# Kernel tuning notes

Hardware: AMD Instinct MI355X
Metric: run time of the kernel (lower is better)

## Reference

```python
import jax, jax.numpy as jnp
import numpy as np

V = 128      # vocab size (pad=0, sos=1, eos=2)
E = 128      # embed_dim == LSTM hidden
L = 2        # rnn_layers
B = 8192     # batch (num_samples)
T = 128      # token sequence length incl. sos/eos
PAD, SOS, EOS = 0, 1, 2


def setup_inputs() -> dict:
    key = jax.random.key(0)
    ks = jax.random.split(key, 9)
    s = 1.0 / np.sqrt(E)
    state = jax.random.normal(ks[0], (B, E), dtype=jnp.float32)
    tokens = jax.random.randint(ks[1], (B, T), 3, V)
    tokens = tokens.at[:, 0].set(SOS).at[:, -1].set(EOS)
    tok_embed = jax.random.normal(ks[2], (V, E), dtype=jnp.float32)
    W_ih = jax.random.uniform(ks[3], (L, 4 * E, E), minval=-s, maxval=s, dtype=jnp.float32)
    W_hh = jax.random.uniform(ks[4], (L, 4 * E, E), minval=-s, maxval=s, dtype=jnp.float32)
    b_ih = jax.random.uniform(ks[5], (L, 4 * E), minval=-s, maxval=s, dtype=jnp.float32)
    b_hh = jax.random.uniform(ks[6], (L, 4 * E), minval=-s, maxval=s, dtype=jnp.float32)
    W_out = jax.random.uniform(ks[7], (V, E), minval=-s, maxval=s, dtype=jnp.float32)
    b_out = jax.random.uniform(ks[8], (V,), minval=-s, maxval=s, dtype=jnp.float32)
    return {"state": state, "tokens": tokens, "tok_embed": tok_embed,
            "W_ih": W_ih, "W_hh": W_hh, "b_ih": b_ih, "b_hh": b_hh,
            "W_out": W_out, "b_out": b_out}


def _lstm(x, h0, c0, W_ih, W_hh, b_ih, b_hh):
    # x: [T, B, E] time-major; h0/c0: [L, B, E]. Gate order i,f,g,o (torch).
    n_layers = W_ih.shape[0]
    hs, cs = [], []
    for l in range(n_layers):
        Wih, Whh = W_ih[l], W_hh[l]
        b = b_ih[l] + b_hh[l]
        def step(carry, xt, Wih=Wih, Whh=Whh, b=b):
            h, c = carry
            g = xt @ Wih.T + h @ Whh.T + b            # [B, 4E]
            i, f, gg, o = jnp.split(g, 4, axis=-1)
            c = jax.nn.sigmoid(f) * c + jax.nn.sigmoid(i) * jnp.tanh(gg)
            h = jax.nn.sigmoid(o) * jnp.tanh(c)
            return (h, c), h
        (h, c), x = jax.lax.scan(step, (h0[l], c0[l]), x)
        hs.append(h)
        cs.append(c)
    return x, jnp.stack(hs), jnp.stack(cs)


def reference(state, tokens, tok_embed, W_ih, W_hh, b_ih, b_hh, W_out, b_out):
    b, e = state.shape
    n_layers = W_ih.shape[0]
    zeros = jnp.zeros((n_layers, b, e), dtype=state.dtype)
    # get_init_state: one-step LSTM over state.unsqueeze(0)
    _, h0, c0 = _lstm(state[None], zeros, zeros, W_ih, W_hh, b_ih, b_hh)
    # get_likelihood (all sequences same length -> dense, no pad tokens)
    x = tok_embed[tokens.T]                               # [T, B, E]
    out, _, _ = _lstm(x, h0, c0, W_ih, W_hh, b_ih, b_hh)  # [T, B, E]
    logits = out[:-1] @ W_out.T + b_out                   # [T-1, B, V]
    targets = tokens.T[1:]                                # [T-1, B]
    lp = jax.nn.log_softmax(logits, axis=-1)
    nll = -jnp.take_along_axis(lp, targets[..., None], axis=-1)[..., 0]
    mask = (targets != PAD).astype(nll.dtype)             # ignore_index=pad
    ll = -jnp.sum(nll * mask, axis=0)[:, None]            # [B, 1]
    return ll
```

## Files before the change

### kernel.cpp

```cpp
#include <hip/hip_runtime.h>
#include <hip/hip_bf16.h>


typedef __bf16 bf16x8 __attribute__((ext_vector_type(8)));
typedef __bf16 bf16x4 __attribute__((ext_vector_type(4)));
typedef float  f32x4  __attribute__((ext_vector_type(4)));

#define LOG2E 1.4426950408889634f
#define LN2   0.6931471805599453f

static __device__ __bf16 g_emb1[128 * 512];

__device__ __forceinline__ float frcp(float x) {
#if __has_builtin(__builtin_amdgcn_rcpf)
  return __builtin_amdgcn_rcpf(x);
#else
  return 1.0f / x;
#endif
}
__device__ __forceinline__ float fexp2(float x) {
#if __has_builtin(__builtin_amdgcn_exp2f)
  return __builtin_amdgcn_exp2f(x);
#else
  return exp2f(x);
#endif
}
__device__ __forceinline__ float flog2(float x) {
#if __has_builtin(__builtin_amdgcn_logf)
  return __builtin_amdgcn_logf(x);
#else
  return log2f(x);
#endif
}

__global__ void prep_emb1(const float* __restrict__ emb, const float* __restrict__ Wih,
                          const float* __restrict__ bih, const float* __restrict__ bhh) {
  __shared__ float embS[128 * 128];
  __shared__ float wS[32 * 128];
  const int tid = threadIdx.x, bc = blockIdx.x;
  for (int i = tid; i < 128 * 32; i += 512) ((f32x4*)embS)[i] = ((const f32x4*)emb)[i];
  for (int i = tid; i < 32 * 32; i += 512)
    ((f32x4*)wS)[i] = ((const f32x4*)(Wih + bc * 32 * 128))[i];
  __syncthreads();
  const int v = tid & 127, c0 = (tid >> 7) * 8;
  const int rot = v & 31;
#pragma unroll
  for (int j = 0; j < 8; ++j) {
    int c = c0 + j;
    float s = 0.f;
    for (int k = 0; k < 128; ++k) {
      int kk = (k + rot) & 127;
      s += embS[v * 128 + kk] * wS[c * 128 + kk];
    }
    int col = bc * 32 + c;
    float sc = ((col >> 7) == 2) ? 2.0f * LOG2E : LOG2E;
    g_emb1[v * 512 + col] = (__bf16)((s + bih[col] + bhh[col]) * sc);
  }
}

__global__ __launch_bounds__(512, 2) void lstm_ll(
    const float* __restrict__ state, const int* __restrict__ tokens,
    const float* __restrict__ W_ih, const float* __restrict__ W_hh,
    const float* __restrict__ b_ih, const float* __restrict__ b_hh,
    const float* __restrict__ W_out, const float* __restrict__ b_out,
    float* __restrict__ out) {
  __shared__ __align__(16) __bf16 wih2L[512 * 128];
  __shared__ __align__(16) __bf16 h1L[2][32 * 128];
  __shared__ __align__(16) __bf16 h2L[32 * 128];
  __shared__ unsigned char tokL[128][32];
  __shared__ float wsum[8][32];
  __shared__ float llL[32];

  const int tid  = threadIdx.x;
  const int w    = tid >> 6;
  const int lane = tid & 63;
  const int lr   = lane & 15;
  const int lh   = lane >> 4;
  const int b0   = blockIdx.x * 32;
  const int col  = w * 16 + lr;
  const int koff = lh * 8;
  const int e0   = w * 16 + lh * 4;
  const float gscA[4] = {LOG2E, LOG2E, 2.0f * LOG2E, LOG2E};
  const int sw = (lr & 7) << 3;

  for (int i = tid; i < 512 * 16; i += 512) {
    int row = i >> 4, e = (i & 15) * 8;
    const float* p = W_ih + 512 * 128 + row * 128 + e;
    float sc = gscA[row >> 7];
    f32x4 x0 = *(const f32x4*)p, x1 = *(const f32x4*)(p + 4);
    bf16x8 v;
#pragma unroll
    for (int j = 0; j < 4; ++j) { v[j] = (__bf16)(x0[j] * sc); v[4 + j] = (__bf16)(x1[j] * sc); }
    *(bf16x8*)(wih2L + row * 128 + (e ^ ((row & 7) << 3))) = v;
  }
  for (int i = tid; i < 32 * 128; i += 512) {
    int r = i & 31, t = i >> 5;
    tokL[t][r] = (unsigned char)tokens[(b0 + r) * 128 + t];
  }
  if (tid < 32) llL[tid] = 0.0f;

  auto ldw8s = [&](const float* p, float sc) -> bf16x8 {
    f32x4 x0 = *(const f32x4*)p, x1 = *(const f32x4*)(p + 4);
    bf16x8 v;
#pragma unroll
    for (int j = 0; j < 4; ++j) { v[j] = (__bf16)(x0[j] * sc); v[4 + j] = (__bf16)(x1[j] * sc); }
    return v;
  };

  bf16x8 whh1[4][4], whh2[4][4], woutF[4];
#pragma unroll
  for (int kc = 0; kc < 4; ++kc) {
#pragma unroll
    for (int gg = 0; gg < 4; ++gg) {
      whh1[kc][gg] = ldw8s(W_hh + (gg * 128 + col) * 128 + kc * 32 + koff, gscA[gg]);
      whh2[kc][gg] = ldw8s(W_hh + 512 * 128 + (gg * 128 + col) * 128 + kc * 32 + koff, gscA[gg]);
    }
    woutF[kc] = ldw8s(W_out + col * 128 + kc * 32 + koff, LOG2E);
  }
  f32x4 bias2v4[4], bo4;
#pragma unroll
  for (int gg = 0; gg < 4; ++gg)
#pragma unroll
    for (int j = 0; j < 4; ++j)
      bias2v4[gg][j] = (b_ih[512 + gg * 128 + e0 + j] + b_hh[512 + gg * 128 + e0 + j]) * gscA[gg];
#pragma unroll
  for (int j = 0; j < 4; ++j) bo4[j] = b_out[e0 + j] * LOG2E;

  float c1[2][4] = {}, c2[2][4] = {};

  auto ldB = [&](const __bf16* buf, int nf, int kc) -> bf16x8 {
    return *(const bf16x8*)(buf + (nf * 16 + lr) * 128 + ((kc * 32 + koff) ^ sw));
  };

  f32x4 acc[4][2];
  auto zacc = [&]() {
#pragma unroll
    for (int gg = 0; gg < 4; ++gg)
#pragma unroll
      for (int nf = 0; nf < 2; ++nf) acc[gg][nf] = f32x4{0.f, 0.f, 0.f, 0.f};
  };

  auto elem = [&](const f32x4* b4, float (&c)[2][4], __bf16* hout) {
#pragma unroll
    for (int nf = 0; nf < 2; ++nf) {
      bf16x4 hp;
#pragma unroll
      for (int j = 0; j < 4; ++j) {
        float gi = acc[0][nf][j] + b4[0][j];
        float gf = acc[1][nf][j] + b4[1][j];
        float gc = acc[2][nf][j] + b4[2][j];
        float go = acc[3][nf][j] + b4[3][j];
        float sf = frcp(1.f + fexp2(-gf));
        float si = frcp(1.f + fexp2(-gi));
        float tg = 1.f - 2.f * frcp(fexp2(gc) + 1.f);
        float cc = sf * c[nf][j] + si * tg;
        c[nf][j] = cc;
        float so = frcp(1.f + fexp2(-go));
        float tc = 1.f - 2.f * frcp(fexp2(2.f * LOG2E * cc) + 1.f);
        hp[j] = (__bf16)(so * tc);
      }
      int b = nf * 16 + lr;
      *(bf16x4*)(hout + b * 128 + (e0 ^ ((b & 7) << 3))) = hp;
    }
  };
  const f32x4 zf4 = {0.f, 0.f, 0.f, 0.f};
  const f32x4 zb4[4] = {zf4, zf4, zf4, zf4};

  __syncthreads();

  bf16x4 gv[2][4];
  auto gather = [&](int t) {
#pragma unroll
    for (int nf = 0; nf < 2; ++nf) {
      int tk = (int)tokL[t][nf * 16 + lr];
      const __bf16* pp = g_emb1 + tk * 512 + e0;
#pragma unroll
      for (int gg = 0; gg < 4; ++gg) gv[nf][gg] = *(const bf16x4*)(pp + gg * 128);
    }
  };
  gather(0);

  {
    zacc();
#pragma unroll
    for (int kc = 0; kc < 4; ++kc) {
      bf16x8 s0 = ldw8s(state + (size_t)(b0 + lr) * 128 + kc * 32 + koff, 1.0f);
      bf16x8 s1 = ldw8s(state + (size_t)(b0 + 16 + lr) * 128 + kc * 32 + koff, 1.0f);
#pragma unroll
      for (int gg = 0; gg < 4; ++gg) {
        bf16x8 a = ldw8s(W_ih + (gg * 128 + col) * 128 + kc * 32 + koff, gscA[gg]);
        acc[gg][0] = __builtin_amdgcn_mfma_f32_16x16x32_bf16(a, s0, acc[gg][0], 0, 0, 0);
        acc[gg][1] = __builtin_amdgcn_mfma_f32_16x16x32_bf16(a, s1, acc[gg][1], 0, 0, 0);
      }
    }
    f32x4 bias1v4[4];
#pragma unroll
    for (int gg = 0; gg < 4; ++gg)
#pragma unroll
      for (int j = 0; j < 4; ++j)
        bias1v4[gg][j] = (b_ih[gg * 128 + e0 + j] + b_hh[gg * 128 + e0 + j]) * gscA[gg];
    elem(bias1v4, c1, h1L[0]);
    __syncthreads();
    zacc();
#pragma unroll
    for (int kc = 0; kc < 4; ++kc) {
      bf16x8 x0 = ldB(h1L[0], 0, kc), x1 = ldB(h1L[0], 1, kc);
#pragma unroll
      for (int gg = 0; gg < 4; ++gg) {
        bf16x8 a = *(const bf16x8*)(wih2L + (gg * 128 + col) * 128 + ((kc * 32 + koff) ^ sw));
        acc[gg][0] = __builtin_amdgcn_mfma_f32_16x16x32_bf16(a, x0, acc[gg][0], 0, 0, 0);
        acc[gg][1] = __builtin_amdgcn_mfma_f32_16x16x32_bf16(a, x1, acc[gg][1], 0, 0, 0);
      }
    }
    elem(bias2v4, c2, h2L);
    __syncthreads();
  }

  f32x4 lvA, lvB;

#pragma unroll 1
  for (int t = 0; t <= 127; ++t) {
    const bool act = (t < 127), pend = (t > 0);
    const __bf16* h1p = h1L[t & 1];
    __bf16* h1c = h1L[(t & 1) ^ 1];

    if (pend) {
      f32x4 la0 = zf4, la1 = zf4;
#pragma unroll
      for (int kc = 0; kc < 4; ++kc) {
        bf16x8 y0 = ldB(h2L, 0, kc), y1 = ldB(h2L, 1, kc);
        la0 = __builtin_amdgcn_mfma_f32_16x16x32_bf16(woutF[kc], y0, la0, 0, 0, 0);
        la1 = __builtin_amdgcn_mfma_f32_16x16x32_bf16(woutF[kc], y1, la1, 0, 0, 0);
      }
      lvA = la0 + bo4;
      lvB = la1 + bo4;
    }
    if (act) {
      zacc();
#pragma unroll
      for (int kc = 0; kc < 4; ++kc) {
        bf16x8 p0 = ldB(h1p, 0, kc), p1 = ldB(h1p, 1, kc);
#pragma unroll
        for (int gg = 0; gg < 4; ++gg) {
          acc[gg][0] = __builtin_amdgcn_mfma_f32_16x16x32_bf16(whh1[kc][gg], p0, acc[gg][0], 0, 0, 0);
          acc[gg][1] = __builtin_amdgcn_mfma_f32_16x16x32_bf16(whh1[kc][gg], p1, acc[gg][1], 0, 0, 0);
        }
      }
#pragma unroll
      for (int nf = 0; nf < 2; ++nf)
#pragma unroll
        for (int gg = 0; gg < 4; ++gg)
#pragma unroll
          for (int j = 0; j < 4; ++j) acc[gg][nf][j] += (float)gv[nf][gg][j];
    }
    if (pend) {
      float s0 = fexp2(lvA[0]) + fexp2(lvA[1]) + fexp2(lvA[2]) + fexp2(lvA[3]);
      float s1 = fexp2(lvB[0]) + fexp2(lvB[1]) + fexp2(lvB[2]) + fexp2(lvB[3]);
      s0 += __shfl_xor(s0, 16); s0 += __shfl_xor(s0, 32);
      s1 += __shfl_xor(s1, 16); s1 += __shfl_xor(s1, 32);
      if (lh == 0) { wsum[w][lr] = s0; wsum[w][16 + lr] = s1; }
    }
    if (act) elem(zb4, c1, h1c);
    __syncthreads();

    if (act) {
      if (t + 1 < 127) gather(t + 1);
      zacc();
#pragma unroll
      for (int kc = 0; kc < 4; ++kc) {
        bf16x8 x0 = ldB(h1c, 0, kc), x1 = ldB(h1c, 1, kc);
        bf16x8 y0 = ldB(h2L, 0, kc), y1 = ldB(h2L, 1, kc);
#pragma unroll
        for (int gg = 0; gg < 4; ++gg) {
          bf16x8 a = *(const bf16x8*)(wih2L + (gg * 128 + col) * 128 + ((kc * 32 + koff) ^ sw));
          acc[gg][0] = __builtin_amdgcn_mfma_f32_16x16x32_bf16(a, x0, acc[gg][0], 0, 0, 0);
          acc[gg][1] = __builtin_amdgcn_mfma_f32_16x16x32_bf16(a, x1, acc[gg][1], 0, 0, 0);
          acc[gg][0] = __builtin_amdgcn_mfma_f32_16x16x32_bf16(whh2[kc][gg], y0, acc[gg][0], 0, 0, 0);
          acc[gg][1] = __builtin_amdgcn_mfma_f32_16x16x32_bf16(whh2[kc][gg], y1, acc[gg][1], 0, 0, 0);
        }
      }
    }
    if (pend) {
#pragma unroll
      for (int nf = 0; nf < 2; ++nf) {
        int r = nf * 16 + lr;
        int tgt = (int)tokL[t][r];
        if ((tgt >> 4) == w && ((tgt >> 2) & 3) == lh) {
          int j = tgt & 3;
          const f32x4& lv = nf ? lvB : lvA;
          float lvs = (j & 2) ? ((j & 1) ? lv[3] : lv[2]) : ((j & 1) ? lv[1] : lv[0]);
          float S = 0.f;
#pragma unroll
          for (int ww = 0; ww < 8; ++ww) S += wsum[ww][r];
          llL[r] += lvs - flog2(S);
        }
      }
    }
    __syncthreads();

    if (act) elem(bias2v4, c2, h2L);
    __syncthreads();
  }

  if (tid < 32) out[b0 + tid] = llL[tid] * LN2;
}

extern "C" void kernel_launch(void* const* d_in, const int* in_sizes, int n_in,
                              void* d_out, int out_size, void* d_ws, size_t ws_size,
                              hipStream_t stream) {
  const float* state  = (const float*)d_in[0];
  const int*   tokens = (const int*)d_in[1];
  const float* emb    = (const float*)d_in[2];
  const float* Wih    = (const float*)d_in[3];
  const float* Whh    = (const float*)d_in[4];
  const float* bih    = (const float*)d_in[5];
  const float* bhh    = (const float*)d_in[6];
  const float* Wout   = (const float*)d_in[7];
  const float* bout   = (const float*)d_in[8];
  float* out = (float*)d_out;

  prep_emb1<<<16, 512, 0, stream>>>(emb, Wih, bih, bhh);
  lstm_ll<<<256, 512, 0, stream>>>(state, tokens, Wih, Whh, bih, bhh, Wout, bout, out);
}
```

Before: 1.128 ms.

## Reschedule LSTM time loop to two barriers per step and rotate-swizzle LDS

Restructures the per-timestep loop into a skewed pipeline. Layer-2 elementwise, softmax partial sums and layer-1 recurrence now share one barrier phase, and the layer-2 GEMM is fused with the output-logit GEMM so both read the h2 tile once. This drops the number of __syncthreads per step from three to two and overlaps independent work. It also replaces the XOR LDS swizzle with a row-rotation swizzle over 16 rows to cut bank conflicts. The pipeline adds an extra loop iteration and shifts token indexing, which raises the risk of off-by-one errors.

```diff
diff --git a/kernel.cpp b/kernel.cpp
--- a/kernel.cpp
+++ b/kernel.cpp
@@ -31,6 +31,10 @@
 #else
   return log2f(x);
 #endif
+}
+
+__device__ __forceinline__ int hoff(int row, int e) {
+  return row * 128 + ((e + ((row & 15) << 3)) & 127);
 }
 
 __global__ void prep_emb1(const float* __restrict__ emb, const float* __restrict__ Wih,
@@ -81,7 +85,6 @@
   const int koff = lh * 8;
   const int e0   = w * 16 + lh * 4;
   const float gscA[4] = {LOG2E, LOG2E, 2.0f * LOG2E, LOG2E};
-  const int sw = (lr & 7) << 3;
 
   for (int i = tid; i < 512 * 16; i += 512) {
     int row = i >> 4, e = (i & 15) * 8;
@@ -91,7 +94,7 @@
     bf16x8 v;
 #pragma unroll
     for (int j = 0; j < 4; ++j) { v[j] = (__bf16)(x0[j] * sc); v[4 + j] = (__bf16)(x1[j] * sc); }
-    *(bf16x8*)(wih2L + row * 128 + (e ^ ((row & 7) << 3))) = v;
+    *(bf16x8*)(wih2L + hoff(row, e)) = v;
   }
   for (int i = tid; i < 32 * 128; i += 512) {
     int r = i & 31, t = i >> 5;
@@ -129,7 +132,7 @@
   float c1[2][4] = {}, c2[2][4] = {};
 
   auto ldB = [&](const __bf16* buf, int nf, int kc) -> bf16x8 {
-    return *(const bf16x8*)(buf + (nf * 16 + lr) * 128 + ((kc * 32 + koff) ^ sw));
+    return *(const bf16x8*)(buf + hoff(nf * 16 + lr, kc * 32 + koff));
   };
 
   f32x4 acc[4][2];
@@ -160,7 +163,7 @@
         hp[j] = (__bf16)(so * tc);
       }
       int b = nf * 16 + lr;
-      *(bf16x4*)(hout + b * 128 + (e0 ^ ((b & 7) << 3))) = hp;
+      *(bf16x4*)(hout + hoff(b, e0)) = hp;
     }
   };
   const f32x4 zf4 = {0.f, 0.f, 0.f, 0.f};
@@ -199,15 +202,15 @@
 #pragma unroll
       for (int j = 0; j < 4; ++j)
         bias1v4[gg][j] = (b_ih[gg * 128 + e0 + j] + b_hh[gg * 128 + e0 + j]) * gscA[gg];
-    elem(bias1v4, c1, h1L[0]);
+    elem(bias1v4, c1, h1L[1]);
     __syncthreads();
     zacc();
 #pragma unroll
     for (int kc = 0; kc < 4; ++kc) {
-      bf16x8 x0 = ldB(h1L[0], 0, kc), x1 = ldB(h1L[0], 1, kc);
+      bf16x8 x0 = ldB(h1L[1], 0, kc), x1 = ldB(h1L[1], 1, kc);
 #pragma unroll
       for (int gg = 0; gg < 4; ++gg) {
-        bf16x8 a = *(const bf16x8*)(wih2L + (gg * 128 + col) * 128 + ((kc * 32 + koff) ^ sw));
+        bf16x8 a = *(const bf16x8*)(wih2L + hoff(gg * 128 + col, kc * 32 + koff));
         acc[gg][0] = __builtin_amdgcn_mfma_f32_16x16x32_bf16(a, x0, acc[gg][0], 0, 0, 0);
         acc[gg][1] = __builtin_amdgcn_mfma_f32_16x16x32_bf16(a, x1, acc[gg][1], 0, 0, 0);
       }
@@ -219,72 +222,47 @@
   f32x4 lvA, lvB;
 
 #pragma unroll 1
-  for (int t = 0; t <= 127; ++t) {
-    const bool act = (t < 127), pend = (t > 0);
-    const __bf16* h1p = h1L[t & 1];
-    __bf16* h1c = h1L[(t & 1) ^ 1];
-
-    if (pend) {
-      f32x4 la0 = zf4, la1 = zf4;
-#pragma unroll
-      for (int kc = 0; kc < 4; ++kc) {
-        bf16x8 y0 = ldB(h2L, 0, kc), y1 = ldB(h2L, 1, kc);
-        la0 = __builtin_amdgcn_mfma_f32_16x16x32_bf16(woutF[kc], y0, la0, 0, 0, 0);
-        la1 = __builtin_amdgcn_mfma_f32_16x16x32_bf16(woutF[kc], y1, la1, 0, 0, 0);
-      }
-      lvA = la0 + bo4;
-      lvB = la1 + bo4;
-    }
-    if (act) {
-      zacc();
-#pragma unroll
-      for (int kc = 0; kc < 4; ++kc) {
-        bf16x8 p0 = ldB(h1p, 0, kc), p1 = ldB(h1p, 1, kc);
-#pragma unroll
-        for (int gg = 0; gg < 4; ++gg) {
-          acc[gg][0] = __builtin_amdgcn_mfma_f32_16x16x32_bf16(whh1[kc][gg], p0, acc[gg][0], 0, 0, 0);
-          acc[gg][1] = __builtin_amdgcn_mfma_f32_16x16x32_bf16(whh1[kc][gg], p1, acc[gg][1], 0, 0, 0);
-        }
-      }
-#pragma unroll
-      for (int nf = 0; nf < 2; ++nf)
-#pragma unroll
-        for (int gg = 0; gg < 4; ++gg)
-#pragma unroll
-          for (int j = 0; j < 4; ++j) acc[gg][nf][j] += (float)gv[nf][gg][j];
-    }
-    if (pend) {
+  for (int t = 0; t <= 128; ++t) {
+    const bool doL1 = (t <= 126);
+    const bool doE2 = (t >= 1) && (t <= 127);
+    const bool doSM = (t >= 2);
+    const bool doLG = (t >= 1) && (t <= 127);
+
+    if (doE2) elem(bias2v4, c2, h2L);
+    if (doSM) {
       float s0 = fexp2(lvA[0]) + fexp2(lvA[1]) + fexp2(lvA[2]) + fexp2(lvA[3]);
       float s1 = fexp2(lvB[0]) + fexp2(lvB[1]) + fexp2(lvB[2]) + fexp2(lvB[3]);
       s0 += __shfl_xor(s0, 16); s0 += __shfl_xor(s0, 32);
       s1 += __shfl_xor(s1, 16); s1 += __shfl_xor(s1, 32);
       if (lh == 0) { wsum[w][lr] = s0; wsum[w][16 + lr] = s1; }
     }
-    if (act) elem(zb4, c1, h1c);
+    if (doL1) {
+      const __bf16* h1p = h1L[(t + 1) & 1];
+      zacc();
+#pragma unroll
+      for (int kc = 0; kc < 4; ++kc) {
+        bf16x8 p0 = ldB(h1p, 0, kc), p1 = ldB(h1p, 1, kc);
+#pragma unroll
+        for (int gg = 0; gg < 4; ++gg) {
+          acc[gg][0] = __builtin_amdgcn_mfma_f32_16x16x32_bf16(whh1[kc][gg], p0, acc[gg][0], 0, 0, 0);
+          acc[gg][1] = __builtin_amdgcn_mfma_f32_16x16x32_bf16(whh1[kc][gg], p1, acc[gg][1], 0, 0, 0);
+        }
+      }
+#pragma unroll
+      for (int nf = 0; nf < 2; ++nf)
+#pragma unroll
+        for (int gg = 0; gg < 4; ++gg)
+#pragma unroll
+          for (int j = 0; j < 4; ++j) acc[gg][nf][j] += (float)gv[nf][gg][j];
+      elem(zb4, c1, h1L[t & 1]);
+    }
     __syncthreads();
 
-    if (act) {
-      if (t + 1 < 127) gather(t + 1);
-      zacc();
-#pragma unroll
-      for (int kc = 0; kc < 4; ++kc) {
-        bf16x8 x0 = ldB(h1c, 0, kc), x1 = ldB(h1c, 1, kc);
-        bf16x8 y0 = ldB(h2L, 0, kc), y1 = ldB(h2L, 1, kc);
-#pragma unroll
-        for (int gg = 0; gg < 4; ++gg) {
-          bf16x8 a = *(const bf16x8*)(wih2L + (gg * 128 + col) * 128 + ((kc * 32 + koff) ^ sw));
-          acc[gg][0] = __builtin_amdgcn_mfma_f32_16x16x32_bf16(a, x0, acc[gg][0], 0, 0, 0);
-          acc[gg][1] = __builtin_amdgcn_mfma_f32_16x16x32_bf16(a, x1, acc[gg][1], 0, 0, 0);
-          acc[gg][0] = __builtin_amdgcn_mfma_f32_16x16x32_bf16(whh2[kc][gg], y0, acc[gg][0], 0, 0, 0);
-          acc[gg][1] = __builtin_amdgcn_mfma_f32_16x16x32_bf16(whh2[kc][gg], y1, acc[gg][1], 0, 0, 0);
-        }
-      }
-    }
-    if (pend) {
+    if (doSM) {
 #pragma unroll
       for (int nf = 0; nf < 2; ++nf) {
         int r = nf * 16 + lr;
-        int tgt = (int)tokL[t][r];
+        int tgt = (int)tokL[t - 1][r];
         if ((tgt >> 4) == w && ((tgt >> 2) & 3) == lh) {
           int j = tgt & 3;
           const f32x4& lv = nf ? lvB : lvA;
@@ -296,9 +274,32 @@
         }
       }
     }
-    __syncthreads();
-
-    if (act) elem(bias2v4, c2, h2L);
+    if (doL1 || doLG) {
+      const __bf16* h1c = h1L[t & 1];
+      f32x4 la0 = zf4, la1 = zf4;
+      if (doL1) zacc();
+#pragma unroll
+      for (int kc = 0; kc < 4; ++kc) {
+        bf16x8 y0 = ldB(h2L, 0, kc), y1 = ldB(h2L, 1, kc);
+        if (doL1) {
+          bf16x8 x0 = ldB(h1c, 0, kc), x1 = ldB(h1c, 1, kc);
+#pragma unroll
+          for (int gg = 0; gg < 4; ++gg) {
+            bf16x8 a = *(const bf16x8*)(wih2L + hoff(gg * 128 + col, kc * 32 + koff));
+            acc[gg][0] = __builtin_amdgcn_mfma_f32_16x16x32_bf16(a, x0, acc[gg][0], 0, 0, 0);
+            acc[gg][1] = __builtin_amdgcn_mfma_f32_16x16x32_bf16(a, x1, acc[gg][1], 0, 0, 0);
+            acc[gg][0] = __builtin_amdgcn_mfma_f32_16x16x32_bf16(whh2[kc][gg], y0, acc[gg][0], 0, 0, 0);
+            acc[gg][1] = __builtin_amdgcn_mfma_f32_16x16x32_bf16(whh2[kc][gg], y1, acc[gg][1], 0, 0, 0);
+          }
+        }
+        if (doLG) {
+          la0 = __builtin_amdgcn_mfma_f32_16x16x32_bf16(woutF[kc], y0, la0, 0, 0, 0);
+          la1 = __builtin_amdgcn_mfma_f32_16x16x32_bf16(woutF[kc], y1, la1, 0, 0, 0);
+        }
+      }
+      if (doLG) { lvA = la0 + bo4; lvB = la1 + bo4; }
+    }
+    if (t <= 125) gather(t + 1);
     __syncthreads();
   }
 
```

After: 1.403 ms. 24.4% more time.

## Stream W_hh and W_out weights from global bf16 copies instead of registers

Applied to the files above, without the earlier changes.

Moves the bf16-converted, pre-scaled W_hh and W_out weights out of per-thread registers into global buffers filled by the prep kernel. Each timestep then reloads them through cache. The goal is lower register pressure, so two 512-thread blocks fit per CU. The LDS swizzle changes from XOR to a rotate-by-row layout, and the gate accumulators are now initialised from the embedding gather rather than added after the MFMAs. The cost is extra global/L2 traffic and load latency on the recurrent critical path every step.

```diff
diff --git a/kernel.cpp b/kernel.cpp
--- a/kernel.cpp
+++ b/kernel.cpp
@@ -10,6 +10,8 @@
 #define LN2   0.6931471805599453f
 
 static __device__ __bf16 g_emb1[128 * 512];
+static __device__ __bf16 g_woutbf[128 * 128];
+static __device__ __bf16 g_whhbf[2 * 512 * 128];
 
 __device__ __forceinline__ float frcp(float x) {
 #if __has_builtin(__builtin_amdgcn_rcpf)
@@ -33,14 +35,29 @@
 #endif
 }
 
+__device__ __forceinline__ int hoff(int row, int e) {
+  return row * 128 + ((e + ((row & 15) << 3)) & 127);
+}
+
 __global__ void prep_emb1(const float* __restrict__ emb, const float* __restrict__ Wih,
-                          const float* __restrict__ bih, const float* __restrict__ bhh) {
+                          const float* __restrict__ bih, const float* __restrict__ bhh,
+                          const float* __restrict__ Wout, const float* __restrict__ Whh) {
   __shared__ float embS[128 * 128];
   __shared__ float wS[32 * 128];
   const int tid = threadIdx.x, bc = blockIdx.x;
   for (int i = tid; i < 128 * 32; i += 512) ((f32x4*)embS)[i] = ((const f32x4*)emb)[i];
   for (int i = tid; i < 32 * 32; i += 512)
     ((f32x4*)wS)[i] = ((const f32x4*)(Wih + bc * 32 * 128))[i];
+  {
+    int idx = bc * 512 + tid;
+    g_woutbf[idx * 2]     = (__bf16)(Wout[idx * 2] * LOG2E);
+    g_woutbf[idx * 2 + 1] = (__bf16)(Wout[idx * 2 + 1] * LOG2E);
+  }
+  for (int i = bc * 512 + tid; i < 2 * 512 * 128; i += 16 * 512) {
+    int gate = (i >> 14) & 3;
+    float sc = (gate == 2) ? 2.0f * LOG2E : LOG2E;
+    g_whhbf[i] = (__bf16)(Whh[i] * sc);
+  }
   __syncthreads();
   const int v = tid & 127, c0 = (tid >> 7) * 8;
   const int rot = v & 31;
@@ -60,9 +77,8 @@
 
 __global__ __launch_bounds__(512, 2) void lstm_ll(
     const float* __restrict__ state, const int* __restrict__ tokens,
-    const float* __restrict__ W_ih, const float* __restrict__ W_hh,
-    const float* __restrict__ b_ih, const float* __restrict__ b_hh,
-    const float* __restrict__ W_out, const float* __restrict__ b_out,
+    const float* __restrict__ W_ih, const float* __restrict__ b_ih,
+    const float* __restrict__ b_hh, const float* __restrict__ b_out,
     float* __restrict__ out) {
   __shared__ __align__(16) __bf16 wih2L[512 * 128];
   __shared__ __align__(16) __bf16 h1L[2][32 * 128];
@@ -81,7 +97,6 @@
   const int koff = lh * 8;
   const int e0   = w * 16 + lh * 4;
   const float gscA[4] = {LOG2E, LOG2E, 2.0f * LOG2E, LOG2E};
-  const int sw = (lr & 7) << 3;
 
   for (int i = tid; i < 512 * 16; i += 512) {
     int row = i >> 4, e = (i & 15) * 8;
@@ -91,7 +106,7 @@
     bf16x8 v;
 #pragma unroll
     for (int j = 0; j < 4; ++j) { v[j] = (__bf16)(x0[j] * sc); v[4 + j] = (__bf16)(x1[j] * sc); }
-    *(bf16x8*)(wih2L + row * 128 + (e ^ ((row & 7) << 3))) = v;
+    *(bf16x8*)(wih2L + hoff(row, e)) = v;
   }
   for (int i = tid; i < 32 * 128; i += 512) {
     int r = i & 31, t = i >> 5;
@@ -107,16 +122,6 @@
     return v;
   };
 
-  bf16x8 whh1[4][4], whh2[4][4], woutF[4];
-#pragma unroll
-  for (int kc = 0; kc < 4; ++kc) {
-#pragma unroll
-    for (int gg = 0; gg < 4; ++gg) {
-      whh1[kc][gg] = ldw8s(W_hh + (gg * 128 + col) * 128 + kc * 32 + koff, gscA[gg]);
-      whh2[kc][gg] = ldw8s(W_hh + 512 * 128 + (gg * 128 + col) * 128 + kc * 32 + koff, gscA[gg]);
-    }
-    woutF[kc] = ldw8s(W_out + col * 128 + kc * 32 + koff, LOG2E);
-  }
   f32x4 bias2v4[4], bo4;
 #pragma unroll
   for (int gg = 0; gg < 4; ++gg)
@@ -129,7 +134,7 @@
   float c1[2][4] = {}, c2[2][4] = {};
 
   auto ldB = [&](const __bf16* buf, int nf, int kc) -> bf16x8 {
-    return *(const bf16x8*)(buf + (nf * 16 + lr) * 128 + ((kc * 32 + koff) ^ sw));
+    return *(const bf16x8*)(buf + hoff(nf * 16 + lr, kc * 32 + koff));
   };
 
   f32x4 acc[4][2];
@@ -160,7 +165,7 @@
         hp[j] = (__bf16)(so * tc);
       }
       int b = nf * 16 + lr;
-      *(bf16x4*)(hout + b * 128 + (e0 ^ ((b & 7) << 3))) = hp;
+      *(bf16x4*)(hout + hoff(b, e0)) = hp;
     }
   };
   const f32x4 zf4 = {0.f, 0.f, 0.f, 0.f};
@@ -207,7 +212,7 @@
       bf16x8 x0 = ldB(h1L[0], 0, kc), x1 = ldB(h1L[0], 1, kc);
 #pragma unroll
       for (int gg = 0; gg < 4; ++gg) {
-        bf16x8 a = *(const bf16x8*)(wih2L + (gg * 128 + col) * 128 + ((kc * 32 + koff) ^ sw));
+        bf16x8 a = *(const bf16x8*)(wih2L + hoff(gg * 128 + col, kc * 32 + koff));
         acc[gg][0] = __builtin_amdgcn_mfma_f32_16x16x32_bf16(a, x0, acc[gg][0], 0, 0, 0);
         acc[gg][1] = __builtin_amdgcn_mfma_f32_16x16x32_bf16(a, x1, acc[gg][1], 0, 0, 0);
       }
@@ -228,30 +233,31 @@
       f32x4 la0 = zf4, la1 = zf4;
 #pragma unroll
       for (int kc = 0; kc < 4; ++kc) {
+        bf16x8 wo = *(const bf16x8*)(g_woutbf + col * 128 + kc * 32 + koff);
         bf16x8 y0 = ldB(h2L, 0, kc), y1 = ldB(h2L, 1, kc);
-        la0 = __builtin_amdgcn_mfma_f32_16x16x32_bf16(woutF[kc], y0, la0, 0, 0, 0);
-        la1 = __builtin_amdgcn_mfma_f32_16x16x32_bf16(woutF[kc], y1, la1, 0, 0, 0);
+        la0 = __builtin_amdgcn_mfma_f32_16x16x32_bf16(wo, y0, la0, 0, 0, 0);
+        la1 = __builtin_amdgcn_mfma_f32_16x16x32_bf16(wo, y1, la1, 0, 0, 0);
       }
       lvA = la0 + bo4;
       lvB = la1 + bo4;
     }
     if (act) {
-      zacc();
+#pragma unroll
+      for (int gg = 0; gg < 4; ++gg)
+#pragma unroll
+        for (int nf = 0; nf < 2; ++nf)
+#pragma unroll
+          for (int j = 0; j < 4; ++j) acc[gg][nf][j] = (float)gv[nf][gg][j];
 #pragma unroll
       for (int kc = 0; kc < 4; ++kc) {
         bf16x8 p0 = ldB(h1p, 0, kc), p1 = ldB(h1p, 1, kc);
 #pragma unroll
         for (int gg = 0; gg < 4; ++gg) {
-          acc[gg][0] = __builtin_amdgcn_mfma_f32_16x16x32_bf16(whh1[kc][gg], p0, acc[gg][0], 0, 0, 0);
-          acc[gg][1] = __builtin_amdgcn_mfma_f32_16x16x32_bf16(whh1[kc][gg], p1, acc[gg][1], 0, 0, 0);
+          bf16x8 a = *(const bf16x8*)(g_whhbf + (size_t)(gg * 128 + col) * 128 + kc * 32 + koff);
+          acc[gg][0] = __builtin_amdgcn_mfma_f32_16x16x32_bf16(a, p0, acc[gg][0], 0, 0, 0);
+          acc[gg][1] = __builtin_amdgcn_mfma_f32_16x16x32_bf16(a, p1, acc[gg][1], 0, 0, 0);
         }
       }
-#pragma unroll
-      for (int nf = 0; nf < 2; ++nf)
-#pragma unroll
-        for (int gg = 0; gg < 4; ++gg)
-#pragma unroll
-          for (int j = 0; j < 4; ++j) acc[gg][nf][j] += (float)gv[nf][gg][j];
     }
     if (pend) {
       float s0 = fexp2(lvA[0]) + fexp2(lvA[1]) + fexp2(lvA[2]) + fexp2(lvA[3]);
@@ -272,11 +278,13 @@
         bf16x8 y0 = ldB(h2L, 0, kc), y1 = ldB(h2L, 1, kc);
 #pragma unroll
         for (int gg = 0; gg < 4; ++gg) {
-          bf16x8 a = *(const bf16x8*)(wih2L + (gg * 128 + col) * 128 + ((kc * 32 + koff) ^ sw));
+          bf16x8 a = *(const bf16x8*)(wih2L + hoff(gg * 128 + col, kc * 32 + koff));
+          bf16x8 a2 = *(const bf16x8*)(g_whhbf + 512 * 128 +
+                                       (size_t)(gg * 128 + col) * 128 + kc * 32 + koff);
           acc[gg][0] = __builtin_amdgcn_mfma_f32_16x16x32_bf16(a, x0, acc[gg][0], 0, 0, 0);
           acc[gg][1] = __builtin_amdgcn_mfma_f32_16x16x32_bf16(a, x1, acc[gg][1], 0, 0, 0);
-          acc[gg][0] = __builtin_amdgcn_mfma_f32_16x16x32_bf16(whh2[kc][gg], y0, acc[gg][0], 0, 0, 0);
-          acc[gg][1] = __builtin_amdgcn_mfma_f32_16x16x32_bf16(whh2[kc][gg], y1, acc[gg][1], 0, 0, 0);
+          acc[gg][0] = __builtin_amdgcn_mfma_f32_16x16x32_bf16(a2, y0, acc[gg][0], 0, 0, 0);
+          acc[gg][1] = __builtin_amdgcn_mfma_f32_16x16x32_bf16(a2, y1, acc[gg][1], 0, 0, 0);
         }
       }
     }
@@ -319,6 +327,6 @@
   const float* bout   = (const float*)d_in[8];
   float* out = (float*)d_out;
 
-  prep_emb1<<<16, 512, 0, stream>>>(emb, Wih, bih, bhh);
-  lstm_ll<<<256, 512, 0, stream>>>(state, tokens, Wih, Whh, bih, bhh, Wout, bout, out);
-}
+  prep_emb1<<<16, 512, 0, stream>>>(emb, Wih, bih, bhh, Wout, Whh);
+  lstm_ll<<<256, 512, 0, stream>>>(state, tokens, Wih, bih, bhh, bout, out);
+}
```

Measured after the change: 1.614 ms. 1.43x slower.
